# Optimization experiments

Measured on AMD Instinct MI355X. Metric: run time of the kernel, lower is better.

Reference implementation:

```python
import jax, jax.numpy as jnp
import numpy as np

NUM_CHANNELS = 10
FEAT = 2048
OUT = 2048
BATCH = 4096
BN_EPS = 1e-3  # keras BatchNormalization default


def setup_inputs() -> dict:
    key = jax.random.key(0)
    k1, k2, k3 = jax.random.split(key, 3)
    x = jax.random.normal(k1, (BATCH, NUM_CHANNELS, FEAT), dtype=jnp.float32)
    adjacency = jax.random.normal(k2, (NUM_CHANNELS, NUM_CHANNELS), dtype=jnp.float32)
    limit = np.sqrt(6.0 / (FEAT + OUT))  # glorot_uniform
    kernel = jax.random.uniform(k3, (FEAT, OUT), dtype=jnp.float32, minval=-limit, maxval=limit)
    bias = jnp.zeros((OUT,), dtype=jnp.float32)
    gamma = jnp.ones((OUT,), dtype=jnp.float32)
    beta = jnp.zeros((OUT,), dtype=jnp.float32)
    moving_mean = jnp.zeros((OUT,), dtype=jnp.float32)
    moving_var = jnp.ones((OUT,), dtype=jnp.float32)
    return {"x": x, "adjacency": adjacency, "kernel": kernel, "bias": bias,
            "gamma": gamma, "beta": beta, "moving_mean": moving_mean, "moving_var": moving_var}


def reference(x, adjacency, kernel, bias, gamma, beta, moving_mean, moving_var):
    # DynamicAdjacencyMatrix: symmetric degree normalization + identity
    degree = jnp.maximum(jnp.sum(jnp.abs(adjacency), axis=1, keepdims=True), 1e-8)  # [C,1]
    dinv = degree ** -0.5
    norm_adj = adjacency * dinv * dinv.T + jnp.eye(NUM_CHANNELS, dtype=adjacency.dtype)  # [C,C]
    # GraphConvolution: features @ kernel, then adjacency mixing over channels
    support = jnp.einsum('bcf,fo->bco', x, kernel)          # [B,C,O]
    out = jnp.einsum('ij,bjo->bio', norm_adj, support) + bias
    out = jax.nn.elu(out)
    # BatchNormalization (inference mode, axis=-1) ; dropout is identity in inference
    out = (out - moving_mean) * jax.lax.rsqrt(moving_var + BN_EPS) * gamma + beta
    return out
```

## Files before the change

### kernel.cpp

```cpp
#include <hip/hip_runtime.h>
#include <cstdint>
#include <cstddef>

#define BATCH 4096
#define NCH 10
#define FEAT 2048
#define NOUT 2048
#define MROWS (BATCH * NCH)
#define KP 6144
#define BN_EPS 1e-3f

using u16 = unsigned short;
typedef __attribute__((ext_vector_type(8))) short bf16x8;
typedef __attribute__((ext_vector_type(8))) unsigned short u16x8;
typedef __attribute__((ext_vector_type(4))) float f32x4;

__device__ __forceinline__ u16 f2bf(float f) {
  uint32_t u = __float_as_uint(f);
  u += 0x7FFFu + ((u >> 16) & 1u);
  return (u16)(u >> 16);
}
__device__ __forceinline__ float bf2f(u16 h) {
  return __uint_as_float(((uint32_t)h) << 16);
}

__device__ __forceinline__ void gload16(const u16* g, u16* l) {
  __builtin_amdgcn_global_load_lds(
      (const __attribute__((address_space(1))) void*)g,
      (__attribute__((address_space(3))) void*)l, 16, 0, 0);
}

__global__ void prep_b_kernel(const float* __restrict__ W, u16* __restrict__ bt) {
  __shared__ float tile[32][33];
  int tx = threadIdx.x, ty = threadIdx.y;
  int n0 = blockIdx.x * 32, k0 = blockIdx.y * 32;
#pragma unroll
  for (int r = 0; r < 4; ++r)
    tile[ty + 8 * r][tx] = W[(size_t)(k0 + ty + 8 * r) * NOUT + n0 + tx];
  __syncthreads();
#pragma unroll
  for (int r = 0; r < 4; ++r) {
    int n = n0 + ty + 8 * r;
    int k = k0 + tx;
    float v = tile[tx][ty + 8 * r];
    u16 hi = f2bf(v);
    u16 lo = f2bf(v - bf2f(hi));
    size_t base = (size_t)n * KP;
    bt[base + k] = hi;
    bt[base + 2048 + k] = hi;
    bt[base + 4096 + k] = lo;
  }
}

__global__ void __launch_bounds__(256) premix_kernel(const float* __restrict__ x,
                                                     const float* __restrict__ adj,
                                                     u16* __restrict__ xh, u16* __restrict__ xl) {
  __shared__ float A[NCH * NCH];
  int t = threadIdx.x;
  if (t < NCH * NCH) {
    int i = t / NCH, j = t % NCH;
    float di = 0.f, dj = 0.f;
#pragma unroll
    for (int q = 0; q < NCH; ++q) {
      di += fabsf(adj[i * NCH + q]);
      dj += fabsf(adj[j * NCH + q]);
    }
    di = fmaxf(di, 1e-8f);
    dj = fmaxf(dj, 1e-8f);
    A[t] = adj[i * NCH + j] * rsqrtf(di * dj) + (i == j ? 1.f : 0.f);
  }
  __syncthreads();
  int b = blockIdx.x;
  const float* xb = x + (size_t)b * (NCH * FEAT);
  u16* xhb = xh + (size_t)b * (NCH * FEAT);
  u16* xlb = xl + (size_t)b * (NCH * FEAT);
  float4 v[NCH][2];
#pragma unroll
  for (int j = 0; j < NCH; ++j) {
    const float4* xp = (const float4*)(xb + j * FEAT + t * 8);
    v[j][0] = xp[0];
    v[j][1] = xp[1];
  }
#pragma unroll
  for (int i = 0; i < NCH; ++i) {
    float o[8] = {0.f, 0.f, 0.f, 0.f, 0.f, 0.f, 0.f, 0.f};
#pragma unroll
    for (int j = 0; j < NCH; ++j) {
      float a = A[i * NCH + j];
      o[0] = fmaf(a, v[j][0].x, o[0]);
      o[1] = fmaf(a, v[j][0].y, o[1]);
      o[2] = fmaf(a, v[j][0].z, o[2]);
      o[3] = fmaf(a, v[j][0].w, o[3]);
      o[4] = fmaf(a, v[j][1].x, o[4]);
      o[5] = fmaf(a, v[j][1].y, o[5]);
      o[6] = fmaf(a, v[j][1].z, o[6]);
      o[7] = fmaf(a, v[j][1].w, o[7]);
    }
    u16x8 hv, lv;
#pragma unroll
    for (int e = 0; e < 8; ++e) {
      u16 h = f2bf(o[e]);
      hv[e] = h;
      lv[e] = f2bf(o[e] - bf2f(h));
    }
    *(u16x8*)(xhb + i * FEAT + t * 8) = hv;
    *(u16x8*)(xlb + i * FEAT + t * 8) = lv;
  }
}

__global__ void __launch_bounds__(256, 3) gemm_kernel(
    const u16* __restrict__ xh, const u16* __restrict__ xl,
    const u16* __restrict__ bt, const float* __restrict__ bias,
    const float* __restrict__ gamma, const float* __restrict__ beta,
    const float* __restrict__ mean, const float* __restrict__ var,
    float* __restrict__ out) {
  __shared__ __align__(16) u16 As[128 * 64];
  __shared__ __align__(16) u16 Bs[128 * 64];
  const int tid = threadIdx.x;
  const int w = tid >> 6, l = tid & 63;
  const int wr = w >> 1, wc = w & 1;
  const int wg = blockIdx.x;
  const int swz = (wg & 7) * 640 + (wg >> 3);
  const int m0 = (swz >> 4) * 128;
  const int n0 = (swz & 15) * 128;
  const int srow = w * 8 + (l >> 3);
  const int scol_sw = (((l & 7) ^ ((l >> 3) & 7)) << 3);
  const int l15 = l & 15;

  f32x4 acc[4][4];
#pragma unroll
  for (int i = 0; i < 4; ++i)
#pragma unroll
    for (int j = 0; j < 4; ++j) acc[i][j] = (f32x4){0.f, 0.f, 0.f, 0.f};

  for (int kk = 0; kk < KP / 64; ++kk) {
    const u16* Ab = (kk >= 32 && kk < 64) ? xl : xh;
    const int ak = (kk & 31) * 64;
    __syncthreads();
#pragma unroll
    for (int i = 0; i < 4; ++i) {
      const u16* g = Ab + (size_t)(m0 + i * 32 + srow) * FEAT + ak + scol_sw;
      gload16(g, &As[i * 2048 + w * 512]);
    }
#pragma unroll
    for (int i = 0; i < 4; ++i) {
      const u16* g = bt + (size_t)(n0 + i * 32 + srow) * KP + kk * 64 + scol_sw;
      gload16(g, &Bs[i * 2048 + w * 512]);
    }
    __syncthreads();
#pragma unroll
    for (int kh = 0; kh < 2; ++kh) {
      bf16x8 af[4], bf[4];
#pragma unroll
      for (int i = 0; i < 4; ++i) {
        const int ra = wr * 64 + i * 16 + l15;
        const int ca = ((kh * 4 + (l >> 4)) ^ (ra & 7)) << 3;
        af[i] = *(const bf16x8*)&As[ra * 64 + ca];
      }
#pragma unroll
      for (int j = 0; j < 4; ++j) {
        const int rb = wc * 64 + j * 16 + l15;
        const int cb = ((kh * 4 + (l >> 4)) ^ (rb & 7)) << 3;
        bf[j] = *(const bf16x8*)&Bs[rb * 64 + cb];
      }
#pragma unroll
      for (int i = 0; i < 4; ++i)
#pragma unroll
        for (int j = 0; j < 4; ++j)
          acc[i][j] = __builtin_amdgcn_mfma_f32_16x16x32_bf16(af[i], bf[j], acc[i][j], 0, 0, 0);
    }
  }

  const int r0 = (l >> 4) * 4;
#pragma unroll
  for (int j = 0; j < 4; ++j) {
    const int col = n0 + wc * 64 + j * 16 + l15;
    const float sv = gamma[col] * rsqrtf(var[col] + BN_EPS);
    const float tv = beta[col] - mean[col] * sv;
    const float bv = bias[col];
#pragma unroll
    for (int i = 0; i < 4; ++i) {
      const int row = m0 + wr * 64 + i * 16 + r0;
#pragma unroll
      for (int r = 0; r < 4; ++r) {
        float v = acc[i][j][r] + bv;
        v = v > 0.f ? v : (expf(v) - 1.f);
        out[(size_t)(row + r) * NOUT + col] = fmaf(v, sv, tv);
      }
    }
  }
}

__global__ void naive_kernel(const float* __restrict__ x, const float* __restrict__ adj,
                             const float* __restrict__ W, const float* __restrict__ bias,
                             const float* __restrict__ gamma, const float* __restrict__ beta,
                             const float* __restrict__ mean, const float* __restrict__ var,
                             float* __restrict__ out) {
  __shared__ float A[NCH * NCH];
  int t = threadIdx.x;
  if (t < NCH * NCH) {
    int i = t / NCH, j = t % NCH;
    float di = 0.f, dj = 0.f;
    for (int q = 0; q < NCH; ++q) {
      di += fabsf(adj[i * NCH + q]);
      dj += fabsf(adj[j * NCH + q]);
    }
    di = fmaxf(di, 1e-8f);
    dj = fmaxf(dj, 1e-8f);
    A[t] = adj[i * NCH + j] * rsqrtf(di * dj) + (i == j ? 1.f : 0.f);
  }
  __syncthreads();
  int idx = blockIdx.x * blockDim.x + threadIdx.x;
  int b = idx >> 11, o = idx & (NOUT - 1);
  const float* xb = x + (size_t)b * (NCH * FEAT);
  float sup[NCH];
#pragma unroll
  for (int j = 0; j < NCH; ++j) sup[j] = 0.f;
  for (int f = 0; f < FEAT; ++f) {
    float wv = W[(size_t)f * NOUT + o];
#pragma unroll
    for (int j = 0; j < NCH; ++j) sup[j] = fmaf(xb[j * FEAT + f], wv, sup[j]);
  }
  float sv = gamma[o] * rsqrtf(var[o] + BN_EPS);
  float tv = beta[o] - mean[o] * sv;
  float bv = bias[o];
#pragma unroll
  for (int i = 0; i < NCH; ++i) {
    float v = bv;
#pragma unroll
    for (int j = 0; j < NCH; ++j) v = fmaf(A[i * NCH + j], sup[j], v);
    v = v > 0.f ? v : (expf(v) - 1.f);
    out[((size_t)b * NCH + i) * NOUT + o] = v * sv + tv;
  }
}

extern "C" void kernel_launch(void* const* d_in, const int* in_sizes, int n_in,
                              void* d_out, int out_size, void* d_ws, size_t ws_size,
                              hipStream_t stream) {
  const float* x     = (const float*)d_in[0];
  const float* adj   = (const float*)d_in[1];
  const float* W     = (const float*)d_in[2];
  const float* bias  = (const float*)d_in[3];
  const float* gamma = (const float*)d_in[4];
  const float* beta  = (const float*)d_in[5];
  const float* mean  = (const float*)d_in[6];
  const float* var   = (const float*)d_in[7];
  float* out = (float*)d_out;

  const size_t XH_OFF = 0;
  const size_t XL_OFF = 167772160ull;
  const size_t BT_OFF = XL_OFF + 167772160ull;
  const size_t WS_NEED = BT_OFF + 25165824ull;

  if (ws_size >= WS_NEED) {
    char* ws = (char*)d_ws;
    u16* xhp = (u16*)(ws + XH_OFF);
    u16* xlp = (u16*)(ws + XL_OFF);
    u16* btp = (u16*)(ws + BT_OFF);
    hipLaunchKernelGGL(prep_b_kernel, dim3(64, 64), dim3(32, 8), 0, stream, W, btp);
    hipLaunchKernelGGL(premix_kernel, dim3(BATCH), dim3(256), 0, stream, x, adj, xhp, xlp);
    hipLaunchKernelGGL(gemm_kernel, dim3((MROWS / 128) * (NOUT / 128)), dim3(256), 0, stream,
                       xhp, xlp, btp, bias, gamma, beta, mean, var, out);
  } else {
    hipLaunchKernelGGL(naive_kernel, dim3((BATCH * NOUT) / 256), dim3(256), 0, stream,
                       x, adj, W, bias, gamma, beta, mean, var, out);
  }
}
```

Before: 1.641 ms.

## Restructure GEMM to 256x256 tiles with double-buffered LDS pipeline

Replaces the 128x128 single-buffered GEMM with 256x256 tiles on 512 threads (8 waves, each holding an 8x4 MFMA accumulator). LDS is double-buffered, and global_load_lds staging for the next k-tile is interleaved into four compute phases per tile, ordered with s_waitcnt and barriers and using setprio around the MFMAs. The B workspace is re-laid out so each 64-wide k-group stores hi/hi/lo contiguously to match the interleaved A source order (xh, xl, xh). The aim is to hide global load latency and raise operand reuse, at the cost of higher register pressure and a fragile hand-written wait and barrier schedule.

After: 1.672 ms. About the same (+1.9%).

```diff
diff --git a/kernel.cpp b/kernel.cpp
--- a/kernel.cpp
+++ b/kernel.cpp
@@ -8,6 +8,7 @@
 #define NOUT 2048
 #define MROWS (BATCH * NCH)
 #define KP 6144
+#define NTILES 96
 #define BN_EPS 1e-3f
 
 using u16 = unsigned short;
@@ -29,6 +30,10 @@
       (const __attribute__((address_space(1))) void*)g,
       (__attribute__((address_space(3))) void*)l, 16, 0, 0);
 }
+
+#define BAR() __builtin_amdgcn_s_barrier()
+#define VMW4() asm volatile("s_waitcnt vmcnt(4)" ::: "memory")
+#define VMW0() asm volatile("s_waitcnt vmcnt(0)" ::: "memory")
 
 __global__ void prep_b_kernel(const float* __restrict__ W, u16* __restrict__ bt) {
   __shared__ float tile[32][33];
@@ -45,10 +50,11 @@
     float v = tile[tx][ty + 8 * r];
     u16 hi = f2bf(v);
     u16 lo = f2bf(v - bf2f(hi));
-    size_t base = (size_t)n * KP;
-    bt[base + k] = hi;
-    bt[base + 2048 + k] = hi;
-    bt[base + 4096 + k] = lo;
+    int g = k >> 6, kc = k & 63;
+    size_t base = (size_t)n * KP + (size_t)(3 * g) * 64 + kc;
+    bt[base] = hi;
+    bt[base + 64] = hi;
+    bt[base + 128] = lo;
   }
 }
 
@@ -108,82 +114,129 @@
   }
 }
 
-__global__ void __launch_bounds__(256, 3) gemm_kernel(
+__device__ __forceinline__ void stage_half(const u16* __restrict__ src, int rstride,
+                                           int grow0, int gcol0, u16* ldsbase,
+                                           int w, int l) {
+  int c0 = w * 64 + l;
+  int r0 = c0 >> 3, cc0 = ((c0 & 7) ^ (r0 & 7)) << 3;
+  gload16(src + (size_t)(grow0 + r0) * rstride + gcol0 + cc0, ldsbase + w * 512);
+  int c1 = 512 + c0;
+  int r1 = c1 >> 3, cc1 = ((c1 & 7) ^ (r1 & 7)) << 3;
+  gload16(src + (size_t)(grow0 + r1) * rstride + gcol0 + cc1, ldsbase + 4096 + w * 512);
+}
+
+template <int Q, class StageFn>
+__device__ __forceinline__ void do_phase(const u16* __restrict__ Abuf,
+                                         const u16* __restrict__ Bbuf,
+                                         f32x4 (&acc)[8][4], bf16x8 (&bfr)[4][2],
+                                         int wr, int wc, int l15, int l4,
+                                         StageFn stage, bool vm4, bool vm0) {
+  if (Q == 0) {
+#pragma unroll
+    for (int nf = 0; nf < 4; ++nf)
+#pragma unroll
+      for (int kh = 0; kh < 2; ++kh) {
+        int row = wc * 64 + nf * 16 + l15;
+        bfr[nf][kh] = *(const bf16x8*)&Bbuf[row * 64 + (((kh * 4 + l4) ^ (row & 7)) << 3)];
+      }
+  }
+  bf16x8 af[2][2];
+#pragma unroll
+  for (int mi = 0; mi < 2; ++mi)
+#pragma unroll
+    for (int kh = 0; kh < 2; ++kh) {
+      int row = wr * 128 + (Q * 2 + mi) * 16 + l15;
+      af[mi][kh] = *(const bf16x8*)&Abuf[row * 64 + (((kh * 4 + l4) ^ (row & 7)) << 3)];
+    }
+  stage();
+  BAR();
+  __builtin_amdgcn_s_setprio(1);
+#pragma unroll
+  for (int mi = 0; mi < 2; ++mi)
+#pragma unroll
+    for (int nf = 0; nf < 4; ++nf)
+#pragma unroll
+      for (int kh = 0; kh < 2; ++kh)
+        acc[Q * 2 + mi][nf] = __builtin_amdgcn_mfma_f32_16x16x32_bf16(
+            af[mi][kh], bfr[nf][kh], acc[Q * 2 + mi][nf], 0, 0, 0);
+  __builtin_amdgcn_s_setprio(0);
+  if (vm4) VMW4();
+  if (vm0) VMW0();
+  BAR();
+}
+
+__global__ void __launch_bounds__(512, 2) gemm_kernel(
     const u16* __restrict__ xh, const u16* __restrict__ xl,
     const u16* __restrict__ bt, const float* __restrict__ bias,
     const float* __restrict__ gamma, const float* __restrict__ beta,
     const float* __restrict__ mean, const float* __restrict__ var,
     float* __restrict__ out) {
-  __shared__ __align__(16) u16 As[128 * 64];
-  __shared__ __align__(16) u16 Bs[128 * 64];
+  __shared__ __align__(16) u16 sA[2][16384];
+  __shared__ __align__(16) u16 sB[2][16384];
   const int tid = threadIdx.x;
   const int w = tid >> 6, l = tid & 63;
-  const int wr = w >> 1, wc = w & 1;
+  const int wr = w >> 2, wc = w & 3;
+  const int l15 = l & 15, l4 = l >> 4;
   const int wg = blockIdx.x;
-  const int swz = (wg & 7) * 640 + (wg >> 3);
-  const int m0 = (swz >> 4) * 128;
-  const int n0 = (swz & 15) * 128;
-  const int srow = w * 8 + (l >> 3);
-  const int scol_sw = (((l & 7) ^ ((l >> 3) & 7)) << 3);
-  const int l15 = l & 15;
-
-  f32x4 acc[4][4];
-#pragma unroll
-  for (int i = 0; i < 4; ++i)
+  const int swz = (wg & 7) * 160 + (wg >> 3);
+  const int m0 = (swz >> 3) * 256;
+  const int n0 = (swz & 7) * 256;
+
+  auto asrc = [&](int t) { return (t % 3 == 1) ? xl : xh; };
+  auto acol = [&](int t) { return (t / 3) * 64; };
+#define SA(t, par, h) stage_half(asrc(t), 2048, m0 + (h)*128, acol(t), &sA[par][(h)*8192], w, l)
+#define SB(t, par, h) stage_half(bt, KP, n0 + (h)*128, (t)*64, &sB[par][(h)*8192], w, l)
+
+  f32x4 acc[8][4];
+#pragma unroll
+  for (int i = 0; i < 8; ++i)
 #pragma unroll
     for (int j = 0; j < 4; ++j) acc[i][j] = (f32x4){0.f, 0.f, 0.f, 0.f};
-
-  for (int kk = 0; kk < KP / 64; ++kk) {
-    const u16* Ab = (kk >= 32 && kk < 64) ? xl : xh;
-    const int ak = (kk & 31) * 64;
-    __syncthreads();
-#pragma unroll
-    for (int i = 0; i < 4; ++i) {
-      const u16* g = Ab + (size_t)(m0 + i * 32 + srow) * FEAT + ak + scol_sw;
-      gload16(g, &As[i * 2048 + w * 512]);
-    }
-#pragma unroll
-    for (int i = 0; i < 4; ++i) {
-      const u16* g = bt + (size_t)(n0 + i * 32 + srow) * KP + kk * 64 + scol_sw;
-      gload16(g, &Bs[i * 2048 + w * 512]);
-    }
-    __syncthreads();
-#pragma unroll
-    for (int kh = 0; kh < 2; ++kh) {
-      bf16x8 af[4], bf[4];
-#pragma unroll
-      for (int i = 0; i < 4; ++i) {
-        const int ra = wr * 64 + i * 16 + l15;
-        const int ca = ((kh * 4 + (l >> 4)) ^ (ra & 7)) << 3;
-        af[i] = *(const bf16x8*)&As[ra * 64 + ca];
-      }
-#pragma unroll
-      for (int j = 0; j < 4; ++j) {
-        const int rb = wc * 64 + j * 16 + l15;
-        const int cb = ((kh * 4 + (l >> 4)) ^ (rb & 7)) << 3;
-        bf[j] = *(const bf16x8*)&Bs[rb * 64 + cb];
-      }
-#pragma unroll
-      for (int i = 0; i < 4; ++i)
-#pragma unroll
-        for (int j = 0; j < 4; ++j)
-          acc[i][j] = __builtin_amdgcn_mfma_f32_16x16x32_bf16(af[i], bf[j], acc[i][j], 0, 0, 0);
-    }
-  }
-
-  const int r0 = (l >> 4) * 4;
-#pragma unroll
-  for (int j = 0; j < 4; ++j) {
-    const int col = n0 + wc * 64 + j * 16 + l15;
+  bf16x8 bfr[4][2];
+
+  SB(0, 0, 0); SB(0, 0, 1);
+  SA(0, 0, 0); SA(0, 0, 1);
+  SB(1, 1, 0); SB(1, 1, 1);
+  VMW4();
+  BAR();
+
+  auto nostage = [] {};
+#pragma unroll 1
+  for (int i = 0; i < 47; ++i) {
+    const int t1 = 2 * i + 1, tb = 2 * i + 2, tb2 = 2 * i + 3;
+    do_phase<0>(sA[0], sB[0], acc, bfr, wr, wc, l15, l4, [&] { SA(t1, 1, 0); }, false, false);
+    do_phase<1>(sA[0], sB[0], acc, bfr, wr, wc, l15, l4, [&] { SA(t1, 1, 1); }, false, false);
+    do_phase<2>(sA[0], sB[0], acc, bfr, wr, wc, l15, l4, [&] { SB(tb, 0, 0); }, false, false);
+    do_phase<3>(sA[0], sB[0], acc, bfr, wr, wc, l15, l4, [&] { SB(tb, 0, 1); }, true, false);
+    do_phase<0>(sA[1], sB[1], acc, bfr, wr, wc, l15, l4, [&] { SA(tb, 0, 0); }, false, false);
+    do_phase<1>(sA[1], sB[1], acc, bfr, wr, wc, l15, l4, [&] { SA(tb, 0, 1); }, false, false);
+    do_phase<2>(sA[1], sB[1], acc, bfr, wr, wc, l15, l4, [&] { SB(tb2, 1, 0); }, false, false);
+    do_phase<3>(sA[1], sB[1], acc, bfr, wr, wc, l15, l4, [&] { SB(tb2, 1, 1); }, true, false);
+  }
+  do_phase<0>(sA[0], sB[0], acc, bfr, wr, wc, l15, l4, [&] { SA(95, 1, 0); }, false, false);
+  do_phase<1>(sA[0], sB[0], acc, bfr, wr, wc, l15, l4, [&] { SA(95, 1, 1); }, false, false);
+  do_phase<2>(sA[0], sB[0], acc, bfr, wr, wc, l15, l4, nostage, false, false);
+  do_phase<3>(sA[0], sB[0], acc, bfr, wr, wc, l15, l4, nostage, false, true);
+  do_phase<0>(sA[1], sB[1], acc, bfr, wr, wc, l15, l4, nostage, false, false);
+  do_phase<1>(sA[1], sB[1], acc, bfr, wr, wc, l15, l4, nostage, false, false);
+  do_phase<2>(sA[1], sB[1], acc, bfr, wr, wc, l15, l4, nostage, false, false);
+  do_phase<3>(sA[1], sB[1], acc, bfr, wr, wc, l15, l4, nostage, false, false);
+#undef SA
+#undef SB
+
+  const int r0 = l4 * 4;
+#pragma unroll
+  for (int nf = 0; nf < 4; ++nf) {
+    const int col = n0 + wc * 64 + nf * 16 + l15;
     const float sv = gamma[col] * rsqrtf(var[col] + BN_EPS);
     const float tv = beta[col] - mean[col] * sv;
     const float bv = bias[col];
 #pragma unroll
-    for (int i = 0; i < 4; ++i) {
-      const int row = m0 + wr * 64 + i * 16 + r0;
+    for (int mf = 0; mf < 8; ++mf) {
+      const int row = m0 + wr * 128 + mf * 16 + r0;
 #pragma unroll
       for (int r = 0; r < 4; ++r) {
-        float v = acc[i][j][r] + bv;
+        float v = acc[mf][nf][r] + bv;
         v = v > 0.f ? v : (expf(v) - 1.f);
         out[(size_t)(row + r) * NOUT + col] = fmaf(v, sv, tv);
       }
@@ -259,7 +312,7 @@
     u16* btp = (u16*)(ws + BT_OFF);
     hipLaunchKernelGGL(prep_b_kernel, dim3(64, 64), dim3(32, 8), 0, stream, W, btp);
     hipLaunchKernelGGL(premix_kernel, dim3(BATCH), dim3(256), 0, stream, x, adj, xhp, xlp);
-    hipLaunchKernelGGL(gemm_kernel, dim3((MROWS / 128) * (NOUT / 128)), dim3(256), 0, stream,
+    hipLaunchKernelGGL(gemm_kernel, dim3((MROWS / 256) * (NOUT / 256)), dim3(512), 0, stream,
                        xhp, xlp, btp, bias, gamma, beta, mean, var, out);
   } else {
     hipLaunchKernelGGL(naive_kernel, dim3((BATCH * NOUT) / 256), dim3(256), 0, stream,
```
